# Performance work log

Measured on AMD Instinct MI355X. Metric: run time of the kernel, lower is better.

The kernel has to match this reference:

```python
import jax, jax.numpy as jnp
import numpy as np

B, S, D = 4, 2048, 1024
H, DK, DV = 16, 64, 64


def setup_inputs() -> dict:
    key = jax.random.key(0)
    ks = jax.random.split(key, 12)
    sd = 0.02
    return {
        "input_query": jax.random.normal(ks[0], (B, S, D), jnp.float32),
        "input_key": jax.random.normal(ks[1], (B, S, D), jnp.float32),
        "input_value": jax.random.normal(ks[2], (B, S, D), jnp.float32),
        "Wq": jax.random.normal(ks[3], (H, D, DK), jnp.float32) * sd,
        "bq": jax.random.normal(ks[4], (H, DK), jnp.float32) * sd,
        "Wk": jax.random.normal(ks[5], (H, D, DK), jnp.float32) * sd,
        "bk": jax.random.normal(ks[6], (H, DK), jnp.float32) * sd,
        "Wv": jax.random.normal(ks[7], (H, D, DV), jnp.float32) * sd,
        "bv": jax.random.normal(ks[8], (H, DV), jnp.float32) * sd,
        "Wo": jax.random.normal(ks[9], (H * DV, D), jnp.float32) * sd,
        "bo": jax.random.normal(ks[10], (D,), jnp.float32) * sd,
    }


def reference(input_query, input_key, input_value, Wq, bq, Wk, bk, Wv, bv, Wo, bo):
    # per-head projections, batched over all heads at once
    q = jnp.einsum("bsd,hdk->bhsk", input_query, Wq) + bq[None, :, None, :]
    k = jnp.einsum("bsd,hdk->bhsk", input_key, Wk) + bk[None, :, None, :]
    v = jnp.einsum("bsd,hdv->bhsv", input_value, Wv) + bv[None, :, None, :]
    # NOTE: original code computes self.dk = sqrt(d_k) but never divides by it,
    # so scores are UNSCALED QK^T (faithful to the source).
    score = jnp.einsum("bhqk,bhsk->bhqs", q, k)  # [B,H,S,S]
    score = jax.nn.softmax(score, axis=-1)
    z = jnp.einsum("bhqs,bhsv->bhqv", score, v)  # [B,H,S,DV]
    # concat heads along feature dim (dim=2 in torch) -> [B,S,H*DV]
    z = jnp.transpose(z, (0, 2, 1, 3)).reshape(z.shape[0], z.shape[2], -1)
    return z @ Wo + bo
```

## Files before the change

kernel.cpp:

```cpp
#include <hip/hip_runtime.h>


using short8  = __attribute__((ext_vector_type(8))) short;
using short4_t= __attribute__((ext_vector_type(4))) short;
using floatx4 = __attribute__((ext_vector_type(4))) float;

#define MFMA32(a, b, c) __builtin_amdgcn_mfma_f32_16x16x32_bf16((a), (b), (c), 0, 0, 0)
#define MFMA16(a, b, c) __builtin_amdgcn_mfma_f32_16x16x16bf16_1k((a), (b), (c), 0, 0, 0)

__device__ __forceinline__ void async16(const unsigned short* g, unsigned short* lds_base) {
  __builtin_amdgcn_global_load_lds(
      (const __attribute__((address_space(1))) unsigned int*)g,
      (__attribute__((address_space(3))) unsigned int*)lds_base, 16, 0, 0);
}

__device__ __forceinline__ float bf2f(unsigned short u) {
  union { unsigned int i; float f; } v; v.i = ((unsigned int)u) << 16; return v.f;
}
__device__ __forceinline__ unsigned short f2bf(float f) {
  union { float f; unsigned int i; } v; v.f = f;
  unsigned int r = v.i + 0x7FFFu + ((v.i >> 16) & 1u);
  return (unsigned short)(r >> 16);
}
__device__ __forceinline__ unsigned int fbits(float f) {
  union { float f; unsigned int i; } v; v.f = f; return v.i;
}
__device__ __forceinline__ unsigned short ld_bf(const void* p, size_t idx, int isbf16) {
  return isbf16 ? ((const unsigned short*)p)[idx] : f2bf(((const float*)p)[idx]);
}
__device__ __forceinline__ float ld_f(const void* p, size_t idx, int isbf16) {
  return isbf16 ? bf2f(((const unsigned short*)p)[idx]) : ((const float*)p)[idx];
}

__global__ void detect_dtype(const unsigned int* __restrict__ X,
                             unsigned int* __restrict__ flag) {
  __shared__ int red[256];
  int cnt = 0;
  for (int i = threadIdx.x; i < 4096; i += 256) {
    unsigned int e = (X[i] >> 7) & 0xFFu;
    cnt += (e >= 96u && e <= 160u) ? 1 : 0;
  }
  red[threadIdx.x] = cnt;
  __syncthreads();
  for (int s = 128; s > 0; s >>= 1) {
    if (threadIdx.x < (unsigned)s) red[threadIdx.x] += red[threadIdx.x + s];
    __syncthreads();
  }
  if (threadIdx.x == 0) *flag = (red[0] >= 2560) ? 1u : 0u;
}

__global__ void convert3(const void* __restrict__ X0, const void* __restrict__ X1,
                         const void* __restrict__ X2,
                         unsigned short* __restrict__ Y0, unsigned short* __restrict__ Y1,
                         unsigned short* __restrict__ Y2,
                         int n8, const unsigned int* __restrict__ flagp) {
  const int isbf16 = (int)*flagp;
  const int z = blockIdx.z;
  const void* X = (z == 0) ? X0 : (z == 1) ? X1 : X2;
  unsigned short* Y = (z == 0) ? Y0 : (z == 1) ? Y1 : Y2;
  int i = blockIdx.x * blockDim.x + threadIdx.x;
  if (i >= n8) return;
  if (isbf16) {
    ((uint4*)Y)[i] = ((const uint4*)X)[i];
  } else {
    const float* f = (const float*)X + (size_t)i * 8;
    union { unsigned short u[8]; uint4 v; } t;
#pragma unroll
    for (int j = 0; j < 8; ++j) t.u[j] = f2bf(f[j]);
    ((uint4*)Y)[i] = t.v;
  }
}

__global__ void transpose_w3(const void* __restrict__ W0, const void* __restrict__ W1,
                             const void* __restrict__ W2,
                             unsigned short* __restrict__ T,
                             const unsigned int* __restrict__ flagp) {
  const int isbf16 = (int)*flagp;
  __shared__ unsigned short tile[32][33];
  const int w = blockIdx.z >> 4, hh = blockIdx.z & 15;
  const void* in = (w == 0) ? W0 : (w == 1) ? W1 : W2;
  const size_t boff = (size_t)hh * 1024 * 64;
  unsigned short* op = T + (size_t)w * (1u << 20) + boff;
  const int r0 = blockIdx.y * 32, c0 = blockIdx.x * 32;
#pragma unroll
  for (int i = 0; i < 4; ++i) {
    int r = threadIdx.y + i * 8;
    tile[r][threadIdx.x] = ld_bf(in, boff + (size_t)(r0 + r) * 64 + (c0 + threadIdx.x), isbf16);
  }
  __syncthreads();
#pragma unroll
  for (int i = 0; i < 4; ++i) {
    int c = threadIdx.y + i * 8;
    op[(size_t)(c0 + c) * 1024 + (r0 + threadIdx.x)] = tile[threadIdx.x][c];
  }
}

__global__ void transpose_any(const void* __restrict__ in,
                              unsigned short* __restrict__ out,
                              int R, int C, const unsigned int* __restrict__ flagp) {
  const int isbf16 = (int)*flagp;
  __shared__ unsigned short tile[32][33];
  const int r0 = blockIdx.y * 32, c0 = blockIdx.x * 32;
#pragma unroll
  for (int i = 0; i < 4; ++i) {
    int r = threadIdx.y + i * 8;
    tile[r][threadIdx.x] = ld_bf(in, (size_t)(r0 + r) * C + (c0 + threadIdx.x), isbf16);
  }
  __syncthreads();
#pragma unroll
  for (int i = 0; i < 4; ++i) {
    int c = threadIdx.y + i * 8;
    out[(size_t)(c0 + c) * R + (r0 + threadIdx.x)] = tile[threadIdx.x][c];
  }
}

#define GEMM_MAIN_LOOP(Aq, Btq, Kdim)                                          \
  floatx4 acc[4][4];                                                           \
  _Pragma("unroll") for (int i = 0; i < 4; ++i)                                \
      _Pragma("unroll") for (int j = 0; j < 4; ++j)                            \
          acc[i][j] = (floatx4){0.f, 0.f, 0.f, 0.f};                           \
  const int lrow = lane >> 3, scol = (lane & 7) * 8;                           \
  for (int k0 = 0; k0 < (Kdim); k0 += 64) {                                    \
    __syncthreads();                                                           \
    _Pragma("unroll") for (int r = 0; r < 4; ++r) {                            \
      const int chunk = r * 4 + wave;                                          \
      const int row = chunk * 8 + lrow;                                        \
      async16(&(Aq)[(size_t)(m0 + row) * (Kdim) + k0 + scol],                  \
              &a_lds[(size_t)chunk * 512]);                                    \
      async16(&(Btq)[(size_t)(n0 + row) * (Kdim) + k0 + scol],                 \
              &b_lds[(size_t)chunk * 512]);                                    \
    }                                                                          \
    __syncthreads();                                                           \
    _Pragma("unroll") for (int kk = 0; kk < 2; ++kk) {                         \
      short8 af[4];                                                            \
      _Pragma("unroll") for (int i = 0; i < 4; ++i)                            \
          af[i] = *(const short8*)&a_lds[(wm + i * 16 + ln15) * 64 + kk * 32 + quad * 8]; \
      _Pragma("unroll") for (int j = 0; j < 4; ++j) {                          \
        short8 bf = *(const short8*)&b_lds[(wn + j * 16 + ln15) * 64 + kk * 32 + quad * 8]; \
        _Pragma("unroll") for (int i = 0; i < 4; ++i)                          \
            acc[i][j] = MFMA32(af[i], bf, acc[i][j]);                          \
      }                                                                        \
    }                                                                          \
  }

__global__ __launch_bounds__(256) void gemm_qkv(
    const unsigned short* __restrict__ A0, const unsigned short* __restrict__ A1,
    const unsigned short* __restrict__ A2,
    const unsigned short* __restrict__ BT,
    const void* __restrict__ b0, const void* __restrict__ b1,
    const void* __restrict__ b2,
    unsigned short* __restrict__ Qp, unsigned short* __restrict__ Kp,
    unsigned short* __restrict__ Vt,
    const unsigned int* __restrict__ flagp)
{
  const int isbf16 = (int)*flagp;
  const int z = blockIdx.z;
  const unsigned short* A  = (z == 0) ? A0 : (z == 1) ? A1 : A2;
  const unsigned short* Bt = BT + ((size_t)z << 20);
  const void* bias = (z == 0) ? b0 : (z == 1) ? b1 : b2;
  const int m0 = blockIdx.x * 128, n0 = blockIdx.y * 128;
  const int tid = threadIdx.x, wave = tid >> 6, lane = tid & 63;
  const int ln15 = lane & 15, quad = lane >> 4;
  const int wm = (wave >> 1) * 64, wn = (wave & 1) * 64;
  __shared__ alignas(16) unsigned short a_lds[128 * 64];
  __shared__ alignas(16) unsigned short b_lds[128 * 64];

  GEMM_MAIN_LOOP(A, Bt, 1024)

  if (z < 2) {
    unsigned short* C = z ? Kp : Qp;
#pragma unroll
    for (int j = 0; j < 4; ++j) {
      const int col = n0 + wn + j * 16 + ln15;
      const float bv = ld_f(bias, col, isbf16);
#pragma unroll
      for (int i = 0; i < 4; ++i) {
        const int row = m0 + wm + i * 16 + quad * 4;
#pragma unroll
        for (int r = 0; r < 4; ++r)
          C[(size_t)(row + r) * 1024 + col] = f2bf(acc[i][j][r] + bv);
      }
    }
  } else {
    __syncthreads();
#pragma unroll
    for (int j = 0; j < 4; ++j) {
      const int nl = wn + j * 16 + ln15;
      const float bv = ld_f(bias, n0 + nl, isbf16);
      unsigned short* dst = (nl < 64) ? &a_lds[(size_t)nl * 128]
                                      : &b_lds[(size_t)(nl - 64) * 128];
#pragma unroll
      for (int i = 0; i < 4; ++i) {
        const int ml = wm + i * 16 + quad * 4;
#pragma unroll
        for (int r = 0; r < 4; ++r) dst[ml + r] = f2bf(acc[i][j][r] + bv);
      }
    }
    __syncthreads();
    const int nl = tid >> 1, half = tid & 1;
    const unsigned short* src = (nl < 64) ? &a_lds[(size_t)nl * 128 + half * 64]
                                          : &b_lds[(size_t)(nl - 64) * 128 + half * 64];
    const int bb = m0 >> 11, s0 = m0 & 2047;
    unsigned short* dst = Vt + (size_t)bb * 2048 * 1024 +
                          (size_t)(n0 + nl) * 2048 + s0 + half * 64;
#pragma unroll
    for (int c = 0; c < 8; ++c) *(uint4*)&dst[c * 8] = *(const uint4*)&src[c * 8];
  }
}

__global__ __launch_bounds__(256) void gemm_out(
    const unsigned short* __restrict__ A,
    const unsigned short* __restrict__ Bt,
    const void* __restrict__ bias,
    void* __restrict__ C,
    const unsigned int* __restrict__ flagp)
{
  const int isbf16 = (int)*flagp;
  const int m0 = blockIdx.x * 128, n0 = blockIdx.y * 128;
  const int tid = threadIdx.x, wave = tid >> 6, lane = tid & 63;
  const int ln15 = lane & 15, quad = lane >> 4;
  const int wm = (wave >> 1) * 64, wn = (wave & 1) * 64;
  __shared__ alignas(16) unsigned short a_lds[128 * 64];
  __shared__ alignas(16) unsigned short b_lds[128 * 64];

  GEMM_MAIN_LOOP(A, Bt, 1024)

#pragma unroll
  for (int j = 0; j < 4; ++j) {
    const int col = n0 + wn + j * 16 + ln15;
    const float bv = ld_f(bias, col, isbf16);
#pragma unroll
    for (int i = 0; i < 4; ++i) {
      const int row = m0 + wm + i * 16 + quad * 4;
#pragma unroll
      for (int r = 0; r < 4; ++r) {
        const float val = acc[i][j][r] + bv;
        if (!isbf16) ((float*)C)[(size_t)(row + r) * 1024 + col] = val;
        else ((unsigned short*)C)[(size_t)(row + r) * 1024 + col] = f2bf(val);
      }
    }
  }
}

__global__ __launch_bounds__(256) void attn(
    const unsigned short* __restrict__ Q,
    const unsigned short* __restrict__ K,
    const unsigned short* __restrict__ Vt,
    unsigned short* __restrict__ Z)
{
  const int qt = blockIdx.x, h = blockIdx.y, b = blockIdx.z;
  const int tid = threadIdx.x, wave = tid >> 6, lane = tid & 63;
  const int ln15 = lane & 15, quad = lane >> 4;

  __shared__ alignas(16) char smem[27648];
  unsigned short* q_lds = (unsigned short*)smem;
  unsigned short* k_lds = (unsigned short*)(smem + 9216);
  unsigned short* v_lds = (unsigned short*)(smem + 18432);

  const unsigned short* Qb = Q + ((size_t)(b * 2048 + qt * 64)) * 1024 + h * 64;
  const unsigned short* Kb = K + ((size_t)(b * 2048)) * 1024 + h * 64;
  const unsigned short* Vh = Vt + (size_t)b * 2048 * 1024 + (size_t)h * 64 * 2048;

  const int sr = tid >> 2, sc = (tid & 3) * 16;
  *(uint4*)&q_lds[sr * 72 + sc]     = *(const uint4*)&Qb[(size_t)sr * 1024 + sc];
  *(uint4*)&q_lds[sr * 72 + sc + 8] = *(const uint4*)&Qb[(size_t)sr * 1024 + sc + 8];
  __syncthreads();
  const short8 qf0 = *(const short8*)&q_lds[(wave * 16 + ln15) * 72 + quad * 8];
  const short8 qf1 = *(const short8*)&q_lds[(wave * 16 + ln15) * 72 + 32 + quad * 8];

  floatx4 o_acc[4];
#pragma unroll
  for (int i = 0; i < 4; ++i) o_acc[i] = (floatx4){0.f, 0.f, 0.f, 0.f};
  float l_part = 0.f;

  for (int j0 = 0; j0 < 2048; j0 += 64) {
    __syncthreads();
    *(uint4*)&k_lds[sr * 72 + sc]     = *(const uint4*)&Kb[(size_t)(j0 + sr) * 1024 + sc];
    *(uint4*)&k_lds[sr * 72 + sc + 8] = *(const uint4*)&Kb[(size_t)(j0 + sr) * 1024 + sc + 8];
    *(uint4*)&v_lds[sr * 72 + sc]     = *(const uint4*)&Vh[(size_t)sr * 2048 + j0 + sc];
    *(uint4*)&v_lds[sr * 72 + sc + 8] = *(const uint4*)&Vh[(size_t)sr * 2048 + j0 + sc + 8];
    __syncthreads();

    floatx4 st[4];
#pragma unroll
    for (int nb = 0; nb < 4; ++nb) {
      const short8 kf0 = *(const short8*)&k_lds[(nb * 16 + ln15) * 72 + quad * 8];
      const short8 kf1 = *(const short8*)&k_lds[(nb * 16 + ln15) * 72 + 32 + quad * 8];
      floatx4 t = (floatx4){0.f, 0.f, 0.f, 0.f};
      t = MFMA32(kf0, qf0, t);
      t = MFMA32(kf1, qf1, t);
      st[nb] = t;
    }

    short4_t pb[4];
#pragma unroll
    for (int nb = 0; nb < 4; ++nb) {
      const float p0 = __expf(st[nb][0]), p1 = __expf(st[nb][1]);
      const float p2 = __expf(st[nb][2]), p3 = __expf(st[nb][3]);
      l_part += (p0 + p1) + (p2 + p3);
      union { unsigned int u[2]; short4_t s; } pk;
      pk.u[0] = (fbits(p0) >> 16) | (fbits(p1) & 0xFFFF0000u);
      pk.u[1] = (fbits(p2) >> 16) | (fbits(p3) & 0xFFFF0000u);
      pb[nb] = pk.s;
    }

#pragma unroll
    for (int vb = 0; vb < 4; ++vb) {
#pragma unroll
      for (int nb = 0; nb < 4; ++nb) {
        const short4_t vf =
            *(const short4_t*)&v_lds[(vb * 16 + ln15) * 72 + nb * 16 + quad * 4];
        o_acc[vb] = MFMA16(vf, pb[nb], o_acc[vb]);
      }
    }
  }

  float l = l_part;
  l += __shfl_xor(l, 16);
  l += __shfl_xor(l, 32);
  const float rl = 1.0f / l;

  __syncthreads();
  float* ot = (float*)smem;
#pragma unroll
  for (int vb = 0; vb < 4; ++vb)
#pragma unroll
    for (int r = 0; r < 4; ++r)
      ot[(wave * 16 + ln15) * 66 + vb * 16 + quad * 4 + r] = o_acc[vb][r] * rl;
  __syncthreads();
  const int q = tid >> 2, vg = (tid & 3) * 16;
  union { unsigned short u[16]; uint4 v[2]; } t;
#pragma unroll
  for (int i = 0; i < 16; ++i) t.u[i] = f2bf(ot[q * 66 + vg + i]);
  unsigned short* dst = Z + ((size_t)(b * 2048 + qt * 64 + q)) * 1024 + h * 64 + vg;
  *(uint4*)&dst[0] = t.v[0];
  *(uint4*)&dst[8] = t.v[1];
}

extern "C" void kernel_launch(void* const* d_in, const int* in_sizes, int n_in,
                              void* d_out, int out_size, void* d_ws, size_t ws_size,
                              hipStream_t stream) {
  const void* Xq = d_in[0];
  const void* Xk = d_in[1];
  const void* Xv = d_in[2];
  const void* Wq = d_in[3];
  const void* bq = d_in[4];
  const void* Wk = d_in[5];
  const void* bk = d_in[6];
  const void* Wv = d_in[7];
  const void* bv = d_in[8];
  const void* Wo = d_in[9];
  const void* bo = d_in[10];

  unsigned int*   flag = (unsigned int*)d_ws;
  unsigned short* base = (unsigned short*)d_ws + 128;
  unsigned short* WqT = base;
  unsigned short* WoT = WqT + (3u << 20);
  unsigned short* buf0 = WoT + (1u << 20);
  unsigned short* buf1 = buf0 + (8u << 20);
  unsigned short* buf2 = buf1 + (8u << 20);
  unsigned short* buf3 = buf2 + (8u << 20);
  unsigned short* buf4 = buf3 + (8u << 20);
  unsigned short *Xqc = buf0, *Xkc = buf1, *Xvc = buf2;
  unsigned short *Qp = buf3, *Kp = buf4;
  unsigned short *Vt = buf0;
  unsigned short *Zp = buf2;
  (void)Vt;

  detect_dtype<<<1, 256, 0, stream>>>((const unsigned int*)Xq, flag);

  transpose_w3<<<dim3(2, 32, 48), dim3(32, 8), 0, stream>>>(Wq, Wk, Wv, WqT, flag);
  transpose_any<<<dim3(32, 32), dim3(32, 8), 0, stream>>>(Wo, WoT, 1024, 1024, flag);

  const int n8 = (8 << 20) / 8;
  convert3<<<dim3(n8 / 256, 1, 3), 256, 0, stream>>>(Xq, Xk, Xv, Xqc, Xkc, Xvc, n8, flag);

  unsigned short* buf5 = buf4 + (8u << 20);
  unsigned short* VtR = buf5;

  gemm_qkv<<<dim3(64, 8, 3), 256, 0, stream>>>(Xqc, Xkc, Xvc, WqT, bq, bk, bv,
                                               Qp, Kp, VtR, flag);

  attn<<<dim3(32, 16, 4), 256, 0, stream>>>(Qp, Kp, VtR, Zp);

  gemm_out<<<dim3(64, 8), 256, 0, stream>>>(Zp, WoT, bo, d_out, flag);
}
```

Measured before the change: 427.1 us.

## Process 256 query rows per attention block to reuse K/V tiles across four groups

```diff
diff --git a/kernel.cpp b/kernel.cpp
--- a/kernel.cpp
+++ b/kernel.cpp
@@ -242,36 +242,47 @@
   }
 }
 
-__global__ __launch_bounds__(256) void attn(
+__global__ __launch_bounds__(256, 2) void attn(
     const unsigned short* __restrict__ Q,
     const unsigned short* __restrict__ K,
     const unsigned short* __restrict__ Vt,
     unsigned short* __restrict__ Z)
 {
-  const int qt = blockIdx.x, h = blockIdx.y, b = blockIdx.z;
+  const int qt0 = blockIdx.x * 256, h = blockIdx.y, b = blockIdx.z;
   const int tid = threadIdx.x, wave = tid >> 6, lane = tid & 63;
   const int ln15 = lane & 15, quad = lane >> 4;
 
-  __shared__ alignas(16) char smem[27648];
+  __shared__ alignas(16) char smem[55296];
   unsigned short* q_lds = (unsigned short*)smem;
-  unsigned short* k_lds = (unsigned short*)(smem + 9216);
-  unsigned short* v_lds = (unsigned short*)(smem + 18432);
-
-  const unsigned short* Qb = Q + ((size_t)(b * 2048 + qt * 64)) * 1024 + h * 64;
+  unsigned short* k_lds = (unsigned short*)(smem + 36864);
+  unsigned short* v_lds = (unsigned short*)(smem + 46080);
+
+  const unsigned short* Qb = Q + ((size_t)(b * 2048 + qt0)) * 1024 + h * 64;
   const unsigned short* Kb = K + ((size_t)(b * 2048)) * 1024 + h * 64;
   const unsigned short* Vh = Vt + (size_t)b * 2048 * 1024 + (size_t)h * 64 * 2048;
 
   const int sr = tid >> 2, sc = (tid & 3) * 16;
-  *(uint4*)&q_lds[sr * 72 + sc]     = *(const uint4*)&Qb[(size_t)sr * 1024 + sc];
-  *(uint4*)&q_lds[sr * 72 + sc + 8] = *(const uint4*)&Qb[(size_t)sr * 1024 + sc + 8];
+#pragma unroll
+  for (int i = 0; i < 4; ++i) {
+    const int r = sr + i * 64;
+    *(uint4*)&q_lds[r * 72 + sc]     = *(const uint4*)&Qb[(size_t)r * 1024 + sc];
+    *(uint4*)&q_lds[r * 72 + sc + 8] = *(const uint4*)&Qb[(size_t)r * 1024 + sc + 8];
+  }
   __syncthreads();
-  const short8 qf0 = *(const short8*)&q_lds[(wave * 16 + ln15) * 72 + quad * 8];
-  const short8 qf1 = *(const short8*)&q_lds[(wave * 16 + ln15) * 72 + 32 + quad * 8];
-
-  floatx4 o_acc[4];
-#pragma unroll
-  for (int i = 0; i < 4; ++i) o_acc[i] = (floatx4){0.f, 0.f, 0.f, 0.f};
-  float l_part = 0.f;
+  short8 qf[4][2];
+#pragma unroll
+  for (int g = 0; g < 4; ++g) {
+    const int row = (g * 4 + wave) * 16 + ln15;
+    qf[g][0] = *(const short8*)&q_lds[row * 72 + quad * 8];
+    qf[g][1] = *(const short8*)&q_lds[row * 72 + 32 + quad * 8];
+  }
+
+  floatx4 o_acc[4][4];
+#pragma unroll
+  for (int g = 0; g < 4; ++g)
+#pragma unroll
+    for (int vb = 0; vb < 4; ++vb) o_acc[g][vb] = (floatx4){0.f, 0.f, 0.f, 0.f};
+  float l_part[4] = {0.f, 0.f, 0.f, 0.f};
 
   for (int j0 = 0; j0 < 2048; j0 += 64) {
     __syncthreads();
@@ -281,60 +292,66 @@
     *(uint4*)&v_lds[sr * 72 + sc + 8] = *(const uint4*)&Vh[(size_t)sr * 2048 + j0 + sc + 8];
     __syncthreads();
 
-    floatx4 st[4];
+    short8 kf[4][2];
+    short4_t vf[4][4];
 #pragma unroll
     for (int nb = 0; nb < 4; ++nb) {
-      const short8 kf0 = *(const short8*)&k_lds[(nb * 16 + ln15) * 72 + quad * 8];
-      const short8 kf1 = *(const short8*)&k_lds[(nb * 16 + ln15) * 72 + 32 + quad * 8];
-      floatx4 t = (floatx4){0.f, 0.f, 0.f, 0.f};
-      t = MFMA32(kf0, qf0, t);
-      t = MFMA32(kf1, qf1, t);
-      st[nb] = t;
+      kf[nb][0] = *(const short8*)&k_lds[(nb * 16 + ln15) * 72 + quad * 8];
+      kf[nb][1] = *(const short8*)&k_lds[(nb * 16 + ln15) * 72 + 32 + quad * 8];
     }
-
-    short4_t pb[4];
-#pragma unroll
-    for (int nb = 0; nb < 4; ++nb) {
-      const float p0 = __expf(st[nb][0]), p1 = __expf(st[nb][1]);
-      const float p2 = __expf(st[nb][2]), p3 = __expf(st[nb][3]);
-      l_part += (p0 + p1) + (p2 + p3);
-      union { unsigned int u[2]; short4_t s; } pk;
-      pk.u[0] = (fbits(p0) >> 16) | (fbits(p1) & 0xFFFF0000u);
-      pk.u[1] = (fbits(p2) >> 16) | (fbits(p3) & 0xFFFF0000u);
-      pb[nb] = pk.s;
+#pragma unroll
+    for (int vb = 0; vb < 4; ++vb)
+#pragma unroll
+      for (int nb = 0; nb < 4; ++nb)
+        vf[vb][nb] = *(const short4_t*)&v_lds[(vb * 16 + ln15) * 72 + nb * 16 + quad * 4];
+
+#pragma unroll
+    for (int g = 0; g < 4; ++g) {
+      short4_t pb[4];
+#pragma unroll
+      for (int nb = 0; nb < 4; ++nb) {
+        floatx4 st = (floatx4){0.f, 0.f, 0.f, 0.f};
+        st = MFMA32(kf[nb][0], qf[g][0], st);
+        st = MFMA32(kf[nb][1], qf[g][1], st);
+        const float p0 = __expf(st[0]), p1 = __expf(st[1]);
+        const float p2 = __expf(st[2]), p3 = __expf(st[3]);
+        l_part[g] += (p0 + p1) + (p2 + p3);
+        union { unsigned int u[2]; short4_t s; } pk;
+        pk.u[0] = (fbits(p0) >> 16) | (fbits(p1) & 0xFFFF0000u);
+        pk.u[1] = (fbits(p2) >> 16) | (fbits(p3) & 0xFFFF0000u);
+        pb[nb] = pk.s;
+      }
+#pragma unroll
+      for (int vb = 0; vb < 4; ++vb)
+#pragma unroll
+        for (int nb = 0; nb < 4; ++nb)
+          o_acc[g][vb] = MFMA16(vf[vb][nb], pb[nb], o_acc[g][vb]);
     }
-
-#pragma unroll
-    for (int vb = 0; vb < 4; ++vb) {
-#pragma unroll
-      for (int nb = 0; nb < 4; ++nb) {
-        const short4_t vf =
-            *(const short4_t*)&v_lds[(vb * 16 + ln15) * 72 + nb * 16 + quad * 4];
-        o_acc[vb] = MFMA16(vf, pb[nb], o_acc[vb]);
-      }
-    }
-  }
-
-  float l = l_part;
-  l += __shfl_xor(l, 16);
-  l += __shfl_xor(l, 32);
-  const float rl = 1.0f / l;
+  }
 
   __syncthreads();
   float* ot = (float*)smem;
-#pragma unroll
-  for (int vb = 0; vb < 4; ++vb)
-#pragma unroll
-    for (int r = 0; r < 4; ++r)
-      ot[(wave * 16 + ln15) * 66 + vb * 16 + quad * 4 + r] = o_acc[vb][r] * rl;
-  __syncthreads();
   const int q = tid >> 2, vg = (tid & 3) * 16;
-  union { unsigned short u[16]; uint4 v[2]; } t;
-#pragma unroll
-  for (int i = 0; i < 16; ++i) t.u[i] = f2bf(ot[q * 66 + vg + i]);
-  unsigned short* dst = Z + ((size_t)(b * 2048 + qt * 64 + q)) * 1024 + h * 64 + vg;
-  *(uint4*)&dst[0] = t.v[0];
-  *(uint4*)&dst[8] = t.v[1];
+#pragma unroll
+  for (int g = 0; g < 4; ++g) {
+    float l = l_part[g];
+    l += __shfl_xor(l, 16);
+    l += __shfl_xor(l, 32);
+    const float rl = 1.0f / l;
+#pragma unroll
+    for (int vb = 0; vb < 4; ++vb)
+#pragma unroll
+      for (int r = 0; r < 4; ++r)
+        ot[(wave * 16 + ln15) * 66 + vb * 16 + quad * 4 + r] = o_acc[g][vb][r] * rl;
+    __syncthreads();
+    union { unsigned short u[16]; uint4 v[2]; } t;
+#pragma unroll
+    for (int i = 0; i < 16; ++i) t.u[i] = f2bf(ot[q * 66 + vg + i]);
+    unsigned short* dst = Z + ((size_t)(b * 2048 + qt0 + g * 64 + q)) * 1024 + h * 64 + vg;
+    *(uint4*)&dst[0] = t.v[0];
+    *(uint4*)&dst[8] = t.v[1];
+    __syncthreads();
+  }
 }
 
 extern "C" void kernel_launch(void* const* d_in, const int* in_sizes, int n_in,
@@ -361,11 +378,10 @@
   unsigned short* buf2 = buf1 + (8u << 20);
   unsigned short* buf3 = buf2 + (8u << 20);
   unsigned short* buf4 = buf3 + (8u << 20);
+  unsigned short* buf5 = buf4 + (8u << 20);
   unsigned short *Xqc = buf0, *Xkc = buf1, *Xvc = buf2;
-  unsigned short *Qp = buf3, *Kp = buf4;
-  unsigned short *Vt = buf0;
+  unsigned short *Qp = buf3, *Kp = buf4, *VtR = buf5;
   unsigned short *Zp = buf2;
-  (void)Vt;
 
   detect_dtype<<<1, 256, 0, stream>>>((const unsigned int*)Xq, flag);
 
@@ -375,13 +391,10 @@
   const int n8 = (8 << 20) / 8;
   convert3<<<dim3(n8 / 256, 1, 3), 256, 0, stream>>>(Xq, Xk, Xv, Xqc, Xkc, Xvc, n8, flag);
 
-  unsigned short* buf5 = buf4 + (8u << 20);
-  unsigned short* VtR = buf5;
-
   gemm_qkv<<<dim3(64, 8, 3), 256, 0, stream>>>(Xqc, Xkc, Xvc, WqT, bq, bk, bv,
                                                Qp, Kp, VtR, flag);
 
-  attn<<<dim3(32, 16, 4), 256, 0, stream>>>(Qp, Kp, VtR, Zp);
+  attn<<<dim3(8, 16, 4), 256, 0, stream>>>(Qp, Kp, VtR, Zp);
 
   gemm_out<<<dim3(64, 8), 256, 0, stream>>>(Zp, WoT, bo, d_out, flag);
 }
```

Result: faster. 370.6 us (-13.2%).
